# Performance work log

Measured on AMD Instinct MI355X. Metric: run time of the kernel, lower is better.

The kernel has to match this reference:

```python
import math
import jax, jax.numpy as jnp
import numpy as np

B, NVARS, NPATCH, DIM, HEADS = 4, 22, 64, 512, 8
L = NVARS * NPATCH          # 1408 tokens
HD = DIM // HEADS           # 64
ALPHA = 0.5                 # top-k prune fraction (smallest dropped)
TEMPORAL_K = 3
DIST_THRESH = 0.55

TCP_PAIRS = [('FP1','F7'),('F7','T3'),('T3','T5'),('T5','O1'),('FP2','F8'),('F8','T4'),('T4','T6'),('T6','O2'),('FP1','F3'),('F3','C3'),('C3','P3'),('P3','O1'),('FP2','F4'),('F4','C4'),('C4','P4'),('P4','O2'),('A1','T3'),('T3','C3'),('C3','CZ'),('CZ','C4'),('C4','T4'),('T4','A2')]
_E3D = {'FP1':(-0.31,0.95,0.0),'FP2':(0.31,0.95,0.0),'F7':(-0.81,0.59,0.0),'F3':(-0.55,0.67,0.5),'FZ':(0.0,0.71,0.71),'F4':(0.55,0.67,0.5),'F8':(0.81,0.59,0.0),'T3':(-1.0,0.0,0.0),'C3':(-0.57,0.0,0.82),'CZ':(0.0,0.0,1.0),'C4':(0.57,0.0,0.82),'T4':(1.0,0.0,0.0),'T5':(-0.81,-0.59,0.0),'P3':(-0.55,-0.67,0.5),'PZ':(0.0,-0.71,0.71),'P4':(0.55,-0.67,0.5),'T6':(0.81,-0.59,0.0),'O1':(-0.31,-0.95,0.0),'O2':(0.31,-0.95,0.0),'A1':(-1.05,0.0,-0.3),'A2':(1.05,0.0,-0.3)}


def build_region_masks_np(n_vars=NVARS, N=NPATCH, n_channels=22,
                          thresh=DIST_THRESH, temporal_k=TEMPORAL_K):
    """Vectorized numpy port of build_region_masks -> [L, 3, L] float32."""
    Ltot = n_vars * N
    # channel adjacency from TCP-pair midpoint distances
    pos = np.array([(np.array(_E3D[a]) + np.array(_E3D[b])) / 2.0
                    for a, b in TCP_PAIRS[:n_channels]])            # [C,3]
    d = np.linalg.norm(pos[:, None, :] - pos[None, :, :], axis=-1)  # [C,C]
    ch_adj = (d < thresh).astype(np.float32)
    np.fill_diagonal(ch_adj, 0.0)
    idx = np.arange(Ltot)
    ch, pa = idx // N, idx % N
    same_patch = pa[:, None] == pa[None, :]
    same_ch = ch[:, None] == ch[None, :]
    adj = ch_adj[np.minimum(ch, n_channels - 1)[:, None],
                 np.minimum(ch, n_channels - 1)[None, :]]
    # S: same patch, different (spatially adjacent) channel
    S = (same_patch & ~same_ch).astype(np.float32) * (adj > 0)
    # T: same channel, patch distance in (0, temporal_k], exp decay
    pd = np.abs(pa[:, None] - pa[None, :])
    T = np.where(same_ch & (pd > 0) & (pd <= temporal_k),
                 np.exp(-pd / max(temporal_k, 1)), 0.0).astype(np.float32)
    # ST: everything else (excluding self)
    ST = np.clip(1.0 - np.eye(Ltot, dtype=np.float32) - S - T, 0.0, None)
    return np.stack([S, T, ST], axis=1)  # [L,3,L]


def setup_inputs() -> dict:
    key = jax.random.key(0)
    k1, k2, k3, k4, k5 = jax.random.split(key, 5)
    x = jax.random.normal(k1, (B, L, DIM), dtype=jnp.float32)
    qkv_w = jax.random.normal(k2, (3 * DIM, DIM), dtype=jnp.float32) * 0.02
    proj_w = jax.random.normal(k3, (DIM, DIM), dtype=jnp.float32) * 0.02
    proj_b = jnp.zeros((DIM,), dtype=jnp.float32)
    region_w = jax.random.normal(k4, (HEADS, 3), dtype=jnp.float32) * 0.5
    region_masks = jnp.asarray(build_region_masks_np())  # [L,3,L]
    return {"x": x, "qkv_w": qkv_w, "proj_w": proj_w, "proj_b": proj_b,
            "region_w": region_w, "region_masks": region_masks}


def _attention(x, qkv_w, proj_w, proj_b, region_w, region_masks):
    Bx, Lx, _ = x.shape
    scale = HD ** -0.5
    qkv = jnp.einsum('bld,ed->ble', x, qkv_w)                 # [B,L,3D]
    qkv = qkv.reshape(Bx, Lx, 3, HEADS, HD).transpose(2, 0, 3, 1, 4)
    q, k, v = qkv[0], qkv[1], qkv[2]                          # [B,H,L,hd]
    scores = jnp.einsum('bhld,bhmd->bhlm', q * scale, k)      # [B,H,L,L]
    # region (S/T/ST) bias, per-head learnable mixing
    region_bias = jnp.einsum('hr,lrm->hlm', region_w, region_masks)
    scores = scores + region_bias[None]
    # mask_topk(alpha, largest=False): drop the k smallest entries per row
    k_drop = max(1, int(ALPHA * Lx))
    _, drop_idx = jax.lax.top_k(-scores, k_drop)              # [B,H,L,k]
    bi = jnp.arange(Bx)[:, None, None, None]
    hi = jnp.arange(HEADS)[None, :, None, None]
    li = jnp.arange(Lx)[None, None, :, None]
    keep = jnp.ones_like(scores).at[bi, hi, li, drop_idx].set(0.0)
    scores = jnp.where(keep > 0, scores, jnp.float32(-1e9))
    attn = jax.nn.softmax(scores, axis=-1)
    out = jnp.einsum('bhlm,bhmd->bhld', attn, v)
    out = out.transpose(0, 2, 1, 3).reshape(Bx, Lx, HEADS * HD)
    return jnp.einsum('ble,de->bld', out, proj_w) + proj_b


def reference(x, qkv_w, proj_w, proj_b, region_w, region_masks):
    return _attention(x, qkv_w, proj_w, proj_b, region_w, region_masks)
```

## Files before the change

### kernel.cpp

```cpp
#include <hip/hip_runtime.h>
#include <stdint.h>

#define BATCH 4
#define LTOT  1408
#define HEADS 8
#define HD    64
#define DIMD  512
#define NKEEP 704
#define RBLK  176
#define SCAP  32

#define SADDR(m, r) (((m) << 3) + (((((r) >> 2) ^ (((m) >> 2) & 1))) << 2) + ((r) & 3))

typedef unsigned int uint;
typedef unsigned short ushort;
typedef __attribute__((ext_vector_type(8))) short bf16x8;
typedef __attribute__((ext_vector_type(4))) float f32x4;

__device__ __forceinline__ uint fkey(float f) {
  uint u = __float_as_uint(f);
  return u ^ ((uint)((int)u >> 31) | 0x80000000u);
}

__device__ __forceinline__ void bf16split(float x, ushort& hi, ushort& lo) {
  uint u = __float_as_uint(x);
  uint h = (u + 0x7FFFu + ((u >> 16) & 1u)) & 0xFFFF0000u;
  hi = (ushort)(h >> 16);
  float r = x - __uint_as_float(h);
  uint v = __float_as_uint(r);
  lo = (ushort)((v + 0x7FFFu + ((v >> 16) & 1u)) >> 16);
}

template<int MODE>
__global__ __launch_bounds__(256)
void gemm_k(const float* __restrict__ A, const float* __restrict__ W,
            const float* __restrict__ pb, ushort* __restrict__ QH,
            ushort* __restrict__ QL, ushort* __restrict__ KH,
            ushort* __restrict__ KL, float* __restrict__ C0, int ntiles)
{
  __shared__ float Ast[16][132];
  __shared__ float Bst[16][132];
  const int t  = threadIdx.x;
  const int mt = blockIdx.x / ntiles, nt = blockIdx.x % ntiles;
  const int m0 = mt * 128, n0 = nt * 128;
  const int lr = t >> 2;
  const int lk = (t & 3) << 2;
  const int tr = t >> 4, tc = t & 15;

  float acc[8][8];
#pragma unroll
  for (int i = 0; i < 8; ++i)
#pragma unroll
    for (int j = 0; j < 8; ++j) acc[i][j] = 0.f;

  for (int k0 = 0; k0 < DIMD; k0 += 16) {
#pragma unroll
    for (int hh = 0; hh < 2; ++hh) {
      const int row = lr + hh * 64;
      const float4 av = *(const float4*)(A + (size_t)(m0 + row) * DIMD + k0 + lk);
      Ast[lk + 0][row] = av.x; Ast[lk + 1][row] = av.y;
      Ast[lk + 2][row] = av.z; Ast[lk + 3][row] = av.w;
      const float4 wv = *(const float4*)(W + (size_t)(n0 + row) * DIMD + k0 + lk);
      Bst[lk + 0][row] = wv.x; Bst[lk + 1][row] = wv.y;
      Bst[lk + 2][row] = wv.z; Bst[lk + 3][row] = wv.w;
    }
    __syncthreads();
#pragma unroll
    for (int k = 0; k < 16; ++k) {
      const float4 a0 = *(const float4*)&Ast[k][tr * 8];
      const float4 a1 = *(const float4*)&Ast[k][tr * 8 + 4];
      const float4 b0 = *(const float4*)&Bst[k][tc * 8];
      const float4 b1 = *(const float4*)&Bst[k][tc * 8 + 4];
      const float a[8] = {a0.x,a0.y,a0.z,a0.w,a1.x,a1.y,a1.z,a1.w};
      const float b[8] = {b0.x,b0.y,b0.z,b0.w,b1.x,b1.y,b1.z,b1.w};
#pragma unroll
      for (int i = 0; i < 8; ++i)
#pragma unroll
        for (int j = 0; j < 8; ++j)
          acc[i][j] = fmaf(a[i], b[j], acc[i][j]);
    }
    __syncthreads();
  }

  const int nb = n0 + tc * 8;
  if (MODE == 0) {
    const int which = nb >> 9;
    const int h  = (nb >> 6) & 7;
    const int d0 = nb & 63;
    const float scl = (which == 0) ? 0.125f : 1.0f;
#pragma unroll
    for (int i = 0; i < 8; ++i) {
      const int gm = m0 + tr * 8 + i;
      const int bb = gm / LTOT, ll = gm % LTOT;
      const size_t off = ((size_t)(bb * HEADS + h) * LTOT + ll) * HD + d0;
      if (which == 2) {
        float4 v0 = make_float4(acc[i][0], acc[i][1], acc[i][2], acc[i][3]);
        float4 v1 = make_float4(acc[i][4], acc[i][5], acc[i][6], acc[i][7]);
        *(float4*)(C0 + off) = v0;
        *(float4*)(C0 + off + 4) = v1;
      } else {
        ushort* Hd = (which == 0) ? QH : KH;
        ushort* Ld = (which == 0) ? QL : KL;
        uint hw[4], lw[4];
#pragma unroll
        for (int jp = 0; jp < 4; ++jp) {
          ushort h0, l0v, h1, l1v;
          bf16split(acc[i][2*jp]     * scl, h0, l0v);
          bf16split(acc[i][2*jp + 1] * scl, h1, l1v);
          hw[jp] = (uint)h0 | ((uint)h1 << 16);
          lw[jp] = (uint)l0v | ((uint)l1v << 16);
        }
        *(uint4*)(Hd + off) = make_uint4(hw[0], hw[1], hw[2], hw[3]);
        *(uint4*)(Ld + off) = make_uint4(lw[0], lw[1], lw[2], lw[3]);
      }
    }
  } else {
    const float4 q0 = *(const float4*)(pb + nb);
    const float4 q1 = *(const float4*)(pb + nb + 4);
#pragma unroll
    for (int i = 0; i < 8; ++i) {
      const int gm = m0 + tr * 8 + i;
      float* p = C0 + (size_t)gm * DIMD + nb;
      float4 v0 = make_float4(acc[i][0]+q0.x, acc[i][1]+q0.y, acc[i][2]+q0.z, acc[i][3]+q0.w);
      float4 v1 = make_float4(acc[i][4]+q1.x, acc[i][5]+q1.y, acc[i][6]+q1.z, acc[i][7]+q1.w);
      *(float4*)p = v0;
      *(float4*)(p + 4) = v1;
    }
  }
}

__global__ __launch_bounds__(256)
void sbias_k(const float* __restrict__ masks, int* __restrict__ sIdx,
             float* __restrict__ sCoef, int* __restrict__ sCnt)
{
  const int l    = blockIdx.x * 4 + (threadIdx.x >> 6);
  const int lane = threadIdx.x & 63;
  const unsigned long long ltmask = (1ull << lane) - 1ull;
  const float* Sm = masks + ((size_t)l * 3 + 0) * LTOT;
  const float* Tm = masks + ((size_t)l * 3 + 1) * LTOT;
  int base = 0;
  for (int i = lane; i < LTOT; i += 64) {
    const float sv = Sm[i];
    const float tv = Tm[i];
    const unsigned long long bS = __ballot(sv != 0.f);
    if (sv != 0.f) {
      const int pos = base + __popcll(bS & ltmask);
      if (pos < SCAP) { sIdx[l * SCAP + pos] = (i << 2) | 0; sCoef[l * SCAP + pos] = sv; }
    }
    base += __popcll(bS);
    const unsigned long long bT = __ballot(tv != 0.f);
    if (tv != 0.f) {
      const int pos = base + __popcll(bT & ltmask);
      if (pos < SCAP) { sIdx[l * SCAP + pos] = (i << 2) | 1; sCoef[l * SCAP + pos] = tv; }
    }
    base += __popcll(bT);
    const unsigned long long bD = __ballot(i == l);
    if (i == l) {
      const int pos = base + __popcll(bD & ltmask);
      if (pos < SCAP) { sIdx[l * SCAP + pos] = (i << 2) | 2; sCoef[l * SCAP + pos] = 1.f; }
    }
    base += __popcll(bD);
  }
  if (lane == 0) sCnt[l] = (base < SCAP) ? base : SCAP;
}

__global__ __launch_bounds__(256, 3)
void attn_k(const ushort* __restrict__ QH, const ushort* __restrict__ QL,
            const ushort* __restrict__ KH, const ushort* __restrict__ KL,
            const float* __restrict__ V, const float* __restrict__ rw,
            const int* __restrict__ sIdx, const float* __restrict__ sCoef,
            const int* __restrict__ sCnt, float* __restrict__ AO)
{
  __shared__ float S[LTOT * 8];
  __shared__ uint  U[2080];

  const int t   = threadIdx.x;
  const int bid = (int)((blockIdx.x & 7) * 704 + (blockIdx.x >> 3));
  const int bh = bid / RBLK;
  const int rb = bid % RBLK;
  const int l0 = rb * 8;
  const int b  = bh >> 3, h = bh & 7;

  const float* Vg = V + (size_t)bh * LTOT * HD;
  const int lane = t & 63;
  const int g    = t >> 6;

  {
    int ar = l0 + (lane & 15);
    if (ar >= LTOT) ar = LTOT - 1;
    const size_t qb = ((size_t)bh * LTOT + ar) * HD + 8 * (lane >> 4);
    const bf16x8 aH0 = *(const bf16x8*)(QH + qb);
    const bf16x8 aH1 = *(const bf16x8*)(QH + qb + 32);
    const bf16x8 aL0 = *(const bf16x8*)(QL + qb);
    const bf16x8 aL1 = *(const bf16x8*)(QL + qb + 32);

#pragma unroll 2
    for (int it = 0; it < 22; ++it) {
      const int m = g * 352 + it * 16 + (lane & 15);
      const size_t kb = ((size_t)bh * LTOT + m) * HD + 8 * (lane >> 4);
      const bf16x8 bH0 = *(const bf16x8*)(KH + kb);
      const bf16x8 bH1 = *(const bf16x8*)(KH + kb + 32);
      const bf16x8 bL0 = *(const bf16x8*)(KL + kb);
      const bf16x8 bL1 = *(const bf16x8*)(KL + kb + 32);
      f32x4 acc = {0.f, 0.f, 0.f, 0.f};
      acc = __builtin_amdgcn_mfma_f32_16x16x32_bf16(aH0, bH0, acc, 0, 0, 0);
      acc = __builtin_amdgcn_mfma_f32_16x16x32_bf16(aH1, bH1, acc, 0, 0, 0);
      acc = __builtin_amdgcn_mfma_f32_16x16x32_bf16(aH0, bL0, acc, 0, 0, 0);
      acc = __builtin_amdgcn_mfma_f32_16x16x32_bf16(aH1, bL1, acc, 0, 0, 0);
      acc = __builtin_amdgcn_mfma_f32_16x16x32_bf16(aL0, bH0, acc, 0, 0, 0);
      acc = __builtin_amdgcn_mfma_f32_16x16x32_bf16(aL1, bH1, acc, 0, 0, 0);
      if (lane < 32) {
        *(float4*)&S[m * 8 + 4 * ((lane >> 4) ^ ((m >> 2) & 1))] =
            make_float4(acc[0], acc[1], acc[2], acc[3]);
      }
    }
  }
  __syncthreads();

  {
    const int rr = t >> 5, jj = t & 31;
    const int l  = l0 + rr;
    if (jj < sCnt[l]) {
      const int   e = sIdx[l * SCAP + jj];
      const float c = sCoef[l * SCAP + jj];
      const int   m = e >> 2, ty = e & 3;
      const float w0 = rw[h * 3 + 0], w1 = rw[h * 3 + 1], w2 = rw[h * 3 + 2];
      const float d = (ty == 0) ? (w0 - w2) * c
                    : (ty == 1) ? (w1 - w2) * c
                                : -w2 * c;
      S[SADDR(m, rr)] += d;
    }
  }

  const int r = t >> 5, j = t & 31;
  uint* hist = U;
  uint prefix = 0, rem = NKEEP;
  for (int p = 0; p < 4; ++p) {
    const int shift = 24 - 8 * p;
    const uint himask = (p == 0) ? 0u : (0xFFFFFFFFu << (8 * (4 - p)));
    __syncthreads();
    for (int i = t; i < 16 * 129; i += 256) hist[i] = 0;
    __syncthreads();
    uint* hr = hist + (r * 2 + (j & 1)) * 129;
    for (int i = j; i < LTOT; i += 32) {
      const uint u = fkey(S[SADDR(i, r)]);
      if ((u & himask) == prefix) {
        const uint bin = (u >> shift) & 255u;
        atomicAdd(&hr[bin >> 1], (bin & 1) ? 65536u : 1u);
      }
    }
    __syncthreads();
    uint c = 0;
#pragma unroll
    for (int bb = 0; bb < 8; ++bb) {
      const int bin = j * 8 + bb;
      const uint w = hist[(r*2+0)*129 + (bin>>1)] + hist[(r*2+1)*129 + (bin>>1)];
      c += (bin & 1) ? (w >> 16) : (w & 0xFFFFu);
    }
    uint sfx = c;
#pragma unroll
    for (int off = 1; off < 32; off <<= 1) {
      const uint o = __shfl_down(sfx, off, 32);
      if (j + off < 32) sfx += o;
    }
    const unsigned long long bal = __ballot(sfx >= rem);
    const uint halfb = (uint)(bal >> (t & 32));
    const int gs = 31 - __clz((int)halfb);
    uint above = __shfl(sfx, (gs + 1) & 31, 32);
    if (gs == 31) above = 0;
    uint rem2 = rem - above;
    int selbin = gs * 8;
#pragma unroll
    for (int bb = 7; bb >= 0; --bb) {
      const int bin = gs * 8 + bb;
      const uint w = hist[(r*2+0)*129 + (bin>>1)] + hist[(r*2+1)*129 + (bin>>1)];
      const uint cnt = (bin & 1) ? (w >> 16) : (w & 0xFFFFu);
      if (rem2 <= cnt) { selbin = bin; break; }
      rem2 -= cnt;
    }
    prefix |= ((uint)selbin) << shift;
    rem = rem2;
  }
  const uint T = prefix;

  float mx = -3.0e38f;
  for (int i = j; i < LTOT; i += 32) mx = fmaxf(mx, S[SADDR(i, r)]);
#pragma unroll
  for (int off = 16; off; off >>= 1) mx = fmaxf(mx, __shfl_xor(mx, off, 32));
  float z = 0.f;
  for (int i = j; i < LTOT; i += 32) {
    const float s = S[SADDR(i, r)];
    const float e = (fkey(s) >= T) ? __expf(s - mx) : 0.f;
    z += e;
    S[SADDR(i, r)] = e;
  }
#pragma unroll
  for (int off = 16; off; off >>= 1) z += __shfl_xor(z, off, 32);
  float* rowZ = (float*)&U[2072];
  if (j == 0) rowZ[r] = z;
  __syncthreads();

  {
    float acc[8];
#pragma unroll
    for (int i = 0; i < 8; ++i) acc[i] = 0.f;
    const int mstart = g * (LTOT / 4), mend = mstart + LTOT / 4;
#pragma unroll 4
    for (int m = mstart; m < mend; ++m) {
      const float v = Vg[(size_t)m * HD + lane];
      const int x = ((m >> 2) & 1) << 2;
      const float4 w0 = *(const float4*)&S[m * 8 + x];
      const float4 w1 = *(const float4*)&S[m * 8 + (4 ^ x)];
      acc[0] = fmaf(w0.x, v, acc[0]); acc[1] = fmaf(w0.y, v, acc[1]);
      acc[2] = fmaf(w0.z, v, acc[2]); acc[3] = fmaf(w0.w, v, acc[3]);
      acc[4] = fmaf(w1.x, v, acc[4]); acc[5] = fmaf(w1.y, v, acc[5]);
      acc[6] = fmaf(w1.z, v, acc[6]); acc[7] = fmaf(w1.w, v, acc[7]);
    }
    float* red = (float*)U;
#pragma unroll
    for (int i = 0; i < 8; ++i) red[(g * 8 + i) * 64 + lane] = acc[i];
  }
  __syncthreads();
  {
    float* red = (float*)U;
    float* rowZp = (float*)&U[2072];
    for (int idx = t; idx < 512; idx += 256) {
      const int rr = idx >> 6, ln = idx & 63;
      const float o = (red[rr*64+ln] + red[512 + rr*64+ln] +
                       red[1024 + rr*64+ln] + red[1536 + rr*64+ln]) / rowZp[rr];
      AO[((size_t)b * LTOT + (l0 + rr)) * DIMD + h * HD + ln] = o;
    }
  }
}

extern "C" void kernel_launch(void* const* d_in, const int* in_sizes, int n_in,
                              void* d_out, int out_size, void* d_ws, size_t ws_size,
                              hipStream_t stream)
{
  (void)in_sizes; (void)n_in; (void)out_size; (void)ws_size;
  const float* x  = (const float*)d_in[0];
  const float* qw = (const float*)d_in[1];
  const float* pw = (const float*)d_in[2];
  const float* pb = (const float*)d_in[3];
  const float* rw = (const float*)d_in[4];
  const float* rm = (const float*)d_in[5];
  float* out = (float*)d_out;
  float* ws  = (float*)d_ws;

  const size_t NQ = (size_t)BATCH * HEADS * LTOT * HD;
  ushort* QH = (ushort*)ws;
  ushort* QL = QH + NQ;
  ushort* KH = QH + 2 * NQ;
  ushort* KL = QH + 3 * NQ;
  float*  Vb = ws + 2 * NQ;
  float*  AO = ws + 3 * NQ;
  float*  sCo = ws + 4 * NQ;
  int*    sId = (int*)(ws + 4 * NQ + LTOT * SCAP);
  int*    sCn = (int*)(ws + 4 * NQ + 2 * LTOT * SCAP);

  sbias_k<<<dim3(352), dim3(256), 0, stream>>>(rm, sId, sCo, sCn);
  gemm_k<0><<<dim3(44 * 12), dim3(256), 0, stream>>>(x, qw, nullptr, QH, QL, KH, KL, Vb, 12);
  attn_k<<<dim3(32 * RBLK), dim3(256), 0, stream>>>(QH, QL, KH, KL, Vb, rw, sId, sCo, sCn, AO);
  gemm_k<1><<<dim3(44 * 4), dim3(256), 0, stream>>>(AO, pw, pb, nullptr, nullptr, nullptr, nullptr, out, 4);
}
```

Before: 830.8 us.

## Compute attention P@V with split-bf16 MFMA using transposed V

The QKV GEMM epilogue now writes V transposed per head as bf16 hi/lo halves, replacing the fp32 row-major V. In the attention kernel the score tile becomes row-major, and the softmax weights are stored as packed bf16 hi/lo pairs with an XOR swizzle. P@V then runs on 16x16x32 bf16 MFMAs using three hi/lo product terms instead of a scalar FMA loop over fp32 V. This aims to cut the VALU and global-load cost of the PV stage, at the price of extra split and pack work and a small loss of precision from the three-term bf16 split.

New measurement: 1.005 ms. +21.0%, slower.

```diff
diff --git a/kernel.cpp b/kernel.cpp
--- a/kernel.cpp
+++ b/kernel.cpp
@@ -10,8 +10,6 @@
 #define RBLK  176
 #define SCAP  32
 
-#define SADDR(m, r) (((m) << 3) + (((((r) >> 2) ^ (((m) >> 2) & 1))) << 2) + ((r) & 3))
-
 typedef unsigned int uint;
 typedef unsigned short ushort;
 typedef __attribute__((ext_vector_type(8))) short bf16x8;
@@ -36,7 +34,8 @@
 void gemm_k(const float* __restrict__ A, const float* __restrict__ W,
             const float* __restrict__ pb, ushort* __restrict__ QH,
             ushort* __restrict__ QL, ushort* __restrict__ KH,
-            ushort* __restrict__ KL, float* __restrict__ C0, int ntiles)
+            ushort* __restrict__ KL, ushort* __restrict__ VH,
+            ushort* __restrict__ VL, float* __restrict__ C0, int ntiles)
 {
   __shared__ float Ast[16][132];
   __shared__ float Bst[16][132];
@@ -88,19 +87,31 @@
     const int h  = (nb >> 6) & 7;
     const int d0 = nb & 63;
     const float scl = (which == 0) ? 0.125f : 1.0f;
-#pragma unroll
-    for (int i = 0; i < 8; ++i) {
-      const int gm = m0 + tr * 8 + i;
-      const int bb = gm / LTOT, ll = gm % LTOT;
-      const size_t off = ((size_t)(bb * HEADS + h) * LTOT + ll) * HD + d0;
-      if (which == 2) {
-        float4 v0 = make_float4(acc[i][0], acc[i][1], acc[i][2], acc[i][3]);
-        float4 v1 = make_float4(acc[i][4], acc[i][5], acc[i][6], acc[i][7]);
-        *(float4*)(C0 + off) = v0;
-        *(float4*)(C0 + off + 4) = v1;
-      } else {
-        ushort* Hd = (which == 0) ? QH : KH;
-        ushort* Ld = (which == 0) ? QL : KL;
+    if (which == 2) {
+      const int bb = (m0 + tr * 8) / LTOT, ll0 = (m0 + tr * 8) % LTOT;
+#pragma unroll
+      for (int jp = 0; jp < 8; ++jp) {
+        uint hw[4], lw[4];
+#pragma unroll
+        for (int ip = 0; ip < 4; ++ip) {
+          ushort h0, l0v, h1, l1v;
+          bf16split(acc[2*ip][jp],     h0, l0v);
+          bf16split(acc[2*ip + 1][jp], h1, l1v);
+          hw[ip] = (uint)h0 | ((uint)h1 << 16);
+          lw[ip] = (uint)l0v | ((uint)l1v << 16);
+        }
+        const size_t off = ((size_t)(bb * HEADS + h) * 64 + (d0 + jp)) * LTOT + ll0;
+        *(uint4*)(VH + off) = make_uint4(hw[0], hw[1], hw[2], hw[3]);
+        *(uint4*)(VL + off) = make_uint4(lw[0], lw[1], lw[2], lw[3]);
+      }
+    } else {
+      ushort* Hd = (which == 0) ? QH : KH;
+      ushort* Ld = (which == 0) ? QL : KL;
+#pragma unroll
+      for (int i = 0; i < 8; ++i) {
+        const int gm = m0 + tr * 8 + i;
+        const int bb = gm / LTOT, ll = gm % LTOT;
+        const size_t off = ((size_t)(bb * HEADS + h) * LTOT + ll) * HD + d0;
         uint hw[4], lw[4];
 #pragma unroll
         for (int jp = 0; jp < 4; ++jp) {
@@ -167,11 +178,12 @@
 __global__ __launch_bounds__(256, 3)
 void attn_k(const ushort* __restrict__ QH, const ushort* __restrict__ QL,
             const ushort* __restrict__ KH, const ushort* __restrict__ KL,
-            const float* __restrict__ V, const float* __restrict__ rw,
+            const ushort* __restrict__ VH, const ushort* __restrict__ VL,
+            const float* __restrict__ rw,
             const int* __restrict__ sIdx, const float* __restrict__ sCoef,
             const int* __restrict__ sCnt, float* __restrict__ AO)
 {
-  __shared__ float S[LTOT * 8];
+  __shared__ float S2[8 * LTOT];
   __shared__ uint  U[2080];
 
   const int t   = threadIdx.x;
@@ -181,7 +193,6 @@
   const int l0 = rb * 8;
   const int b  = bh >> 3, h = bh & 7;
 
-  const float* Vg = V + (size_t)bh * LTOT * HD;
   const int lane = t & 63;
   const int g    = t >> 6;
 
@@ -210,8 +221,11 @@
       acc = __builtin_amdgcn_mfma_f32_16x16x32_bf16(aL0, bH0, acc, 0, 0, 0);
       acc = __builtin_amdgcn_mfma_f32_16x16x32_bf16(aL1, bH1, acc, 0, 0, 0);
       if (lane < 32) {
-        *(float4*)&S[m * 8 + 4 * ((lane >> 4) ^ ((m >> 2) & 1))] =
-            make_float4(acc[0], acc[1], acc[2], acc[3]);
+        const int r0 = 4 * (lane >> 4);
+        S2[(r0 + 0) * LTOT + m] = acc[0];
+        S2[(r0 + 1) * LTOT + m] = acc[1];
+        S2[(r0 + 2) * LTOT + m] = acc[2];
+        S2[(r0 + 3) * LTOT + m] = acc[3];
       }
     }
   }
@@ -228,7 +242,7 @@
       const float d = (ty == 0) ? (w0 - w2) * c
                     : (ty == 1) ? (w1 - w2) * c
                                 : -w2 * c;
-      S[SADDR(m, rr)] += d;
+      S2[rr * LTOT + m] += d;
     }
   }
 
@@ -243,7 +257,7 @@
     __syncthreads();
     uint* hr = hist + (r * 2 + (j & 1)) * 129;
     for (int i = j; i < LTOT; i += 32) {
-      const uint u = fkey(S[SADDR(i, r)]);
+      const uint u = fkey(S2[r * LTOT + i]);
       if ((u & himask) == prefix) {
         const uint bin = (u >> shift) & 255u;
         atomicAdd(&hr[bin >> 1], (bin & 1) ? 65536u : 1u);
@@ -284,15 +298,20 @@
   const uint T = prefix;
 
   float mx = -3.0e38f;
-  for (int i = j; i < LTOT; i += 32) mx = fmaxf(mx, S[SADDR(i, r)]);
+  for (int i = j; i < LTOT; i += 32) mx = fmaxf(mx, S2[r * LTOT + i]);
 #pragma unroll
   for (int off = 16; off; off >>= 1) mx = fmaxf(mx, __shfl_xor(mx, off, 32));
   float z = 0.f;
-  for (int i = j; i < LTOT; i += 32) {
-    const float s = S[SADDR(i, r)];
-    const float e = (fkey(s) >= T) ? __expf(s - mx) : 0.f;
-    z += e;
-    S[SADDR(i, r)] = e;
+  {
+    const int xr = (r & 3) << 3;
+    uint* S2u = (uint*)S2;
+    for (int i = j; i < LTOT; i += 32) {
+      const float s = S2[r * LTOT + i];
+      const float e = (fkey(s) >= T) ? __expf(s - mx) : 0.f;
+      z += e;
+      ushort ph, pl; bf16split(e, ph, pl);
+      S2u[r * LTOT + (i ^ xr)] = (uint)ph | ((uint)pl << 16);
+    }
   }
 #pragma unroll
   for (int off = 16; off; off >>= 1) z += __shfl_xor(z, off, 32);
@@ -301,24 +320,48 @@
   __syncthreads();
 
   {
-    float acc[8];
-#pragma unroll
-    for (int i = 0; i < 8; ++i) acc[i] = 0.f;
-    const int mstart = g * (LTOT / 4), mend = mstart + LTOT / 4;
-#pragma unroll 4
-    for (int m = mstart; m < mend; ++m) {
-      const float v = Vg[(size_t)m * HD + lane];
-      const int x = ((m >> 2) & 1) << 2;
-      const float4 w0 = *(const float4*)&S[m * 8 + x];
-      const float4 w1 = *(const float4*)&S[m * 8 + (4 ^ x)];
-      acc[0] = fmaf(w0.x, v, acc[0]); acc[1] = fmaf(w0.y, v, acc[1]);
-      acc[2] = fmaf(w0.z, v, acc[2]); acc[3] = fmaf(w0.w, v, acc[3]);
-      acc[4] = fmaf(w1.x, v, acc[4]); acc[5] = fmaf(w1.y, v, acc[5]);
-      acc[6] = fmaf(w1.z, v, acc[6]); acc[7] = fmaf(w1.w, v, acc[7]);
+    f32x4 acc[4];
+#pragma unroll
+    for (int nt = 0; nt < 4; ++nt) acc[nt] = f32x4{0.f, 0.f, 0.f, 0.f};
+    const int h4 = lane >> 4;
+    const int arow = ((lane & 15) < 8) ? (lane & 15) : 7;
+    const int xr = (arow & 3) << 3;
+    const uint* S2u = (const uint*)S2;
+    const size_t vbase = (size_t)bh * 64 * LTOT;
+    for (int ks = 0; ks < 11; ++ks) {
+      const int mw = g * 352 + ks * 32 + 8 * h4;
+      const int W0 = arow * LTOT + (mw ^ xr);
+      const uint4 ua = *(const uint4*)&S2u[W0];
+      const uint4 ub = *(const uint4*)&S2u[W0 + 4];
+      uint4 ahv, alv;
+      ahv.x = (ua.x & 0xFFFFu) | (ua.y << 16);
+      alv.x = (ua.x >> 16) | (ua.y & 0xFFFF0000u);
+      ahv.y = (ua.z & 0xFFFFu) | (ua.w << 16);
+      alv.y = (ua.z >> 16) | (ua.w & 0xFFFF0000u);
+      ahv.z = (ub.x & 0xFFFFu) | (ub.y << 16);
+      alv.z = (ub.x >> 16) | (ub.y & 0xFFFF0000u);
+      ahv.w = (ub.z & 0xFFFFu) | (ub.w << 16);
+      alv.w = (ub.z >> 16) | (ub.w & 0xFFFF0000u);
+      const bf16x8 aH = *(const bf16x8*)&ahv;
+      const bf16x8 aL = *(const bf16x8*)&alv;
+#pragma unroll
+      for (int nt = 0; nt < 4; ++nt) {
+        const size_t vo = vbase + (size_t)(nt * 16 + (lane & 15)) * LTOT + mw;
+        const bf16x8 bH = *(const bf16x8*)(VH + vo);
+        const bf16x8 bL = *(const bf16x8*)(VL + vo);
+        acc[nt] = __builtin_amdgcn_mfma_f32_16x16x32_bf16(aH, bH, acc[nt], 0, 0, 0);
+        acc[nt] = __builtin_amdgcn_mfma_f32_16x16x32_bf16(aH, bL, acc[nt], 0, 0, 0);
+        acc[nt] = __builtin_amdgcn_mfma_f32_16x16x32_bf16(aL, bH, acc[nt], 0, 0, 0);
+      }
     }
     float* red = (float*)U;
-#pragma unroll
-    for (int i = 0; i < 8; ++i) red[(g * 8 + i) * 64 + lane] = acc[i];
+    if (lane < 32) {
+#pragma unroll
+      for (int nt = 0; nt < 4; ++nt)
+#pragma unroll
+        for (int q = 0; q < 4; ++q)
+          red[g * 512 + (4 * h4 + q) * 64 + nt * 16 + (lane & 15)] = acc[nt][q];
+    }
   }
   __syncthreads();
   {
@@ -352,14 +395,15 @@
   ushort* QL = QH + NQ;
   ushort* KH = QH + 2 * NQ;
   ushort* KL = QH + 3 * NQ;
-  float*  Vb = ws + 2 * NQ;
+  ushort* VH = QH + 4 * NQ;
+  ushort* VL = QH + 5 * NQ;
   float*  AO = ws + 3 * NQ;
   float*  sCo = ws + 4 * NQ;
   int*    sId = (int*)(ws + 4 * NQ + LTOT * SCAP);
   int*    sCn = (int*)(ws + 4 * NQ + 2 * LTOT * SCAP);
 
   sbias_k<<<dim3(352), dim3(256), 0, stream>>>(rm, sId, sCo, sCn);
-  gemm_k<0><<<dim3(44 * 12), dim3(256), 0, stream>>>(x, qw, nullptr, QH, QL, KH, KL, Vb, 12);
-  attn_k<<<dim3(32 * RBLK), dim3(256), 0, stream>>>(QH, QL, KH, KL, Vb, rw, sId, sCo, sCn, AO);
-  gemm_k<1><<<dim3(44 * 4), dim3(256), 0, stream>>>(AO, pw, pb, nullptr, nullptr, nullptr, nullptr, out, 4);
-}
+  gemm_k<0><<<dim3(44 * 12), dim3(256), 0, stream>>>(x, qw, nullptr, QH, QL, KH, KL, VH, VL, nullptr, 12);
+  attn_k<<<dim3(32 * RBLK), dim3(256), 0, stream>>>(QH, QL, KH, KL, VH, VL, rw, sId, sCo, sCn, AO);
+  gemm_k<1><<<dim3(44 * 4), dim3(256), 0, stream>>>(AO, pw, pb, nullptr, nullptr, nullptr, nullptr, nullptr, nullptr, out, 4);
+}
```
